# Performance work log

Measured on AMD Instinct MI355X. Metric: run time of the kernel, lower is better.

## Reference

```python
import jax, jax.numpy as jnp
import numpy as np

# Mamba block hyperparams (canonical: expand=2, d_state=16, d_conv=4, dt_rank=d_model/16)
D_MODEL = 1024
D_INNER = 2 * D_MODEL          # 2048
D_STATE = 16
D_CONV = 4
DT_RANK = D_MODEL // 16        # 64
B, L = 2, 1024


def setup_inputs() -> dict:
    key = jax.random.key(0)
    ks = jax.random.split(key, 12)
    s = lambda fan_in: 1.0 / np.sqrt(fan_in)
    x = jax.random.normal(ks[0], (B, L, D_MODEL), dtype=jnp.float32)
    W_in = jax.random.normal(ks[1], (D_MODEL, 2 * D_INNER), dtype=jnp.float32) * s(D_MODEL)
    conv_w = jax.random.normal(ks[2], (D_INNER, 1, D_CONV), dtype=jnp.float32) * s(D_CONV)
    conv_b = jax.random.normal(ks[3], (D_INNER,), dtype=jnp.float32) * 0.02
    W_xp = jax.random.normal(ks[4], (D_INNER, DT_RANK + 2 * D_STATE), dtype=jnp.float32) * s(D_INNER)
    W_dt = jax.random.normal(ks[5], (DT_RANK, D_INNER), dtype=jnp.float32) * s(DT_RANK)
    # dt bias init so softplus(dt_bias) ~ uniform in [1e-3, 1e-1] (mamba convention)
    dt = jnp.exp(jax.random.uniform(ks[6], (D_INNER,)) * (np.log(0.1) - np.log(1e-3)) + np.log(1e-3))
    dt_bias = dt + jnp.log(-jnp.expm1(-dt))  # inverse softplus
    A_log = jnp.log(jnp.broadcast_to(jnp.arange(1, D_STATE + 1, dtype=jnp.float32), (D_INNER, D_STATE)))
    D_skip = jnp.ones((D_INNER,), dtype=jnp.float32)
    W_out = jax.random.normal(ks[7], (D_INNER, D_MODEL), dtype=jnp.float32) * s(D_INNER)
    return {"x": x, "W_in": W_in, "conv_w": conv_w, "conv_b": conv_b, "W_xp": W_xp,
            "W_dt": W_dt, "dt_bias": dt_bias, "A_log": A_log, "D_skip": D_skip, "W_out": W_out}


def _causal_depthwise_conv(u, conv_w, conv_b):
    # u: [B, E, L], conv_w: [E, 1, K] depthwise, causal (left-pad K-1)
    K = conv_w.shape[-1]
    u = jnp.pad(u, ((0, 0), (0, 0), (K - 1, 0)))
    y = jax.lax.conv_general_dilated(
        u, conv_w, window_strides=(1,), padding='VALID',
        dimension_numbers=('NCH', 'OIH', 'NCH'), feature_group_count=u.shape[1])
    return y + conv_b[None, :, None]


def _selective_scan(u, delta, A, Bm, Cm, D_skip):
    # u, delta: [B,L,E]; A: [E,N]; Bm, Cm: [B,L,N]; D_skip: [E]
    dA = jnp.exp(jnp.einsum('ble,en->blen', delta, A))          # [B,L,E,N]
    dBu = jnp.einsum('ble,bln,ble->blen', delta, Bm, u)          # [B,L,E,N]

    def step(h, inp):
        dA_t, dBu_t, C_t = inp                                    # [B,E,N],[B,E,N],[B,N]
        h = dA_t * h + dBu_t
        y_t = jnp.einsum('ben,bn->be', h, C_t)
        return h, y_t

    h0 = jnp.zeros((u.shape[0], A.shape[0], A.shape[1]), dtype=u.dtype)
    xs = (jnp.swapaxes(dA, 0, 1), jnp.swapaxes(dBu, 0, 1), jnp.swapaxes(Cm, 0, 1))
    _, ys = jax.lax.scan(step, h0, xs)                            # ys: [L,B,E]
    y = jnp.swapaxes(ys, 0, 1)                                    # [B,L,E]
    return y + u * D_skip[None, None, :]


def reference(x, W_in, conv_w, conv_b, W_xp, W_dt, dt_bias, A_log, D_skip, W_out):
    # in_proj and gate split
    xz = x @ W_in                                                 # [B,L,2E]
    xp, z = jnp.split(xz, 2, axis=-1)                             # [B,L,E] each
    # causal depthwise conv + silu
    u = _causal_depthwise_conv(jnp.swapaxes(xp, 1, 2), conv_w, conv_b)
    u = jax.nn.silu(jnp.swapaxes(u, 1, 2))                        # [B,L,E]
    # input-dependent dt, B, C
    x_dbl = u @ W_xp                                              # [B,L,R+2N]
    dt_r, Bm, Cm = jnp.split(x_dbl, [DT_RANK, DT_RANK + D_STATE], axis=-1)
    delta = jax.nn.softplus(dt_r @ W_dt + dt_bias)                # [B,L,E]
    A = -jnp.exp(A_log)                                           # [E,N]
    y = _selective_scan(u, delta, A, Bm, Cm, D_skip)              # [B,L,E]
    # gate and out_proj
    y = y * jax.nn.silu(z)
    return y @ W_out                                              # [B,L,D]
```

## Files before the change

### kernel.cpp

```cpp
#include <hip/hip_runtime.h>
#include <math.h>

#define D_MODEL 1024
#define D_INNER 2048
#define D_STATE 16
#define D_CONV  4
#define DT_RANK 64
#define BB      2
#define LL      1024
#define BL      (BB*LL)
#define CHUNK   16
#define NCHUNK  (LL/CHUNK)
#define KSPLIT  16
#define KS_E    (D_INNER/KSPLIT)

typedef __attribute__((ext_vector_type(8))) short short8;
typedef __attribute__((ext_vector_type(4))) float f32x4;
typedef unsigned short ushort_t;
typedef unsigned int uint_t;

__device__ __forceinline__ float sigmoidf_(float x) { return 1.0f / (1.0f + __expf(-x)); }

__device__ __forceinline__ ushort_t f2bf(float f) {
    uint_t u = __float_as_uint(f);
    uint_t r = (u + 0x7fffu + ((u >> 16) & 1u)) >> 16;
    return (ushort_t)r;
}
__device__ __forceinline__ float bf2f(ushort_t v) {
    return __uint_as_float((uint_t)v << 16);
}

__device__ __forceinline__ void gload_lds16(const void* g, void* l) {
    __builtin_amdgcn_global_load_lds(
        (const __attribute__((address_space(1))) void*)g,
        (__attribute__((address_space(3))) void*)l,
        16, 0, 0);
}

template<int BM, int BN, int SPLIT, int BF0, int BF1>
__global__ __launch_bounds__(256)
void gemm_bf16_t(const ushort_t* __restrict__ A, const ushort_t* __restrict__ Bt,
                 void* __restrict__ C0v, void* __restrict__ C1v,
                 int M, int N, int K, int split) {
    constexpr int WMr = BM / 32;
    constexpr int WNr = BN / 32;
    const int nx = N / BN;
    const int nwg = nx * (M / BM);
    const int wg = ((blockIdx.x & 7) * (nwg >> 3)) + (blockIdx.x >> 3);
    const int row0 = (wg / nx) * BM;
    const int col0 = (wg % nx) * BN;

    __shared__ __align__(16) ushort_t As[BM * 32];
    __shared__ __align__(16) ushort_t Bs[BN * 32];

    const int tid  = threadIdx.x;
    const int lane = tid & 63;
    const int wave = tid >> 6;
    const int wr = wave >> 1, wc = wave & 1;

    f32x4 acc[WMr][WNr];
    #pragma unroll
    for (int m = 0; m < WMr; ++m)
        #pragma unroll
        for (int n = 0; n < WNr; ++n)
            acc[m][n] = (f32x4){0.f, 0.f, 0.f, 0.f};

    const ushort_t* Ablk = A  + (size_t)row0 * K;
    const ushort_t* Bblk = Bt + (size_t)col0 * K;
    const int r_ld  = tid >> 2;
    const int c8_ld = (tid & 3) * 8;

    for (int k0 = 0; k0 < K; k0 += 32) {
        #pragma unroll
        for (int i = 0; i < BM / 64; ++i)
            gload_lds16(Ablk + (size_t)(i * 64 + r_ld) * K + k0 + c8_ld,
                        &As[(i * 64 + wave * 16) * 32]);
        #pragma unroll
        for (int i = 0; i < BN / 64; ++i)
            gload_lds16(Bblk + (size_t)(i * 64 + r_ld) * K + k0 + c8_ld,
                        &Bs[(i * 64 + wave * 16) * 32]);
        __syncthreads();

        short8 af[WMr], bf[WNr];
        const int fr = lane & 15;
        const int kb = (lane >> 4) * 8;
        #pragma unroll
        for (int m = 0; m < WMr; ++m)
            af[m] = *(const short8*)&As[(wr * WMr * 16 + m * 16 + fr) * 32 + kb];
        #pragma unroll
        for (int n = 0; n < WNr; ++n)
            bf[n] = *(const short8*)&Bs[(wc * WNr * 16 + n * 16 + fr) * 32 + kb];

        #pragma unroll
        for (int m = 0; m < WMr; ++m)
            #pragma unroll
            for (int n = 0; n < WNr; ++n)
                acc[m][n] = __builtin_amdgcn_mfma_f32_16x16x32_bf16(
                    af[m], bf[n], acc[m][n], 0, 0, 0);
        __syncthreads();
    }

    const int crow = (lane >> 4) * 4;
    const int ccol = lane & 15;
    const bool second = SPLIT && (col0 >= split);
    const int ldc = second ? (N - split) : (SPLIT ? split : N);
    const int cb  = second ? (col0 - split) : col0;

    #pragma unroll
    for (int m = 0; m < WMr; ++m) {
        #pragma unroll
        for (int n = 0; n < WNr; ++n) {
            size_t base = (size_t)(row0 + wr * WMr * 16 + m * 16 + crow) * ldc
                          + cb + wc * WNr * 16 + n * 16 + ccol;
            if (second) {
                if (BF1) { ushort_t* cp = (ushort_t*)C1v + base;
                    #pragma unroll
                    for (int i = 0; i < 4; ++i) cp[(size_t)i * ldc] = f2bf(acc[m][n][i]);
                } else { float* cp = (float*)C1v + base;
                    #pragma unroll
                    for (int i = 0; i < 4; ++i) cp[(size_t)i * ldc] = acc[m][n][i];
                }
            } else {
                if (BF0) { ushort_t* cp = (ushort_t*)C0v + base;
                    #pragma unroll
                    for (int i = 0; i < 4; ++i) cp[(size_t)i * ldc] = f2bf(acc[m][n][i]);
                } else { float* cp = (float*)C0v + base;
                    #pragma unroll
                    for (int i = 0; i < 4; ++i) cp[(size_t)i * ldc] = acc[m][n][i];
                }
            }
        }
    }
}

__global__ __launch_bounds__(256)
void f32_to_bf16(const float* __restrict__ in, ushort_t* __restrict__ out, int n) {
    int i = (blockIdx.x * 256 + threadIdx.x) * 8;
    if (i + 8 <= n) {
        float4 a = *reinterpret_cast<const float4*>(in + i);
        float4 b = *reinterpret_cast<const float4*>(in + i + 4);
        ushort_t o[8] = {f2bf(a.x), f2bf(a.y), f2bf(a.z), f2bf(a.w),
                         f2bf(b.x), f2bf(b.y), f2bf(b.z), f2bf(b.w)};
        *reinterpret_cast<short8*>(out + i) = *reinterpret_cast<short8*>(o);
    }
}

__global__ __launch_bounds__(256)
void transp_bf16(const float* __restrict__ W, ushort_t* __restrict__ Wt,
                 int R, int C) {
    __shared__ ushort_t tile[32][33];
    int tx = threadIdx.x & 31, ty = threadIdx.x >> 5;
    int r0 = blockIdx.y * 32, c0 = blockIdx.x * 32;
    #pragma unroll
    for (int i = 0; i < 32; i += 8)
        tile[ty + i][tx] = f2bf(W[(size_t)(r0 + ty + i) * C + c0 + tx]);
    __syncthreads();
    #pragma unroll
    for (int i = 0; i < 32; i += 8)
        Wt[(size_t)(c0 + ty + i) * R + r0 + tx] = tile[tx][ty + i];
}

__global__ __launch_bounds__(256)
void gemm_xdbl_convfused(const float* __restrict__ xp, const float* __restrict__ W,
                         const float* __restrict__ conv_w, const float* __restrict__ conv_b,
                         float* __restrict__ part) {
    __shared__ float Ax[16][68];
    __shared__ float Au[16][65];
    __shared__ float Bs[16][96];

    const int tid = threadIdx.x;
    const int m0 = blockIdx.x * 64;
    const int kbase = blockIdx.y * KS_E;
    const int tx = tid & 15;
    const int ty = tid >> 4;
    const bool bhead = (m0 & (LL - 1)) == 0;

    float acc[4][6] = {};

    for (int k0 = 0; k0 < KS_E; k0 += 16) {
        for (int i = tid; i < 67 * 16; i += 256) {
            int r = i >> 4, k = i & 15;
            float v = 0.f;
            if (!(bhead && r < 3))
                v = xp[(size_t)(m0 - 3 + r) * D_INNER + kbase + k0 + k];
            Ax[k][r] = v;
        }
        #pragma unroll
        for (int j = 0; j < 6; ++j) {
            int idx = j * 256 + tid;
            int row = idx / 96, col = idx - row * 96;
            Bs[row][col] = W[(size_t)(kbase + k0 + row) * 96 + col];
        }
        __syncthreads();
        {
            float4 w4 = *(const float4*)&conv_w[(size_t)(kbase + k0 + tx) * 4];
            float cbv = conv_b[kbase + k0 + tx];
            #pragma unroll
            for (int rr = 0; rr < 4; ++rr) {
                int r = ty + rr * 16;
                float a = cbv;
                a = fmaf(w4.x, Ax[tx][r], a);
                a = fmaf(w4.y, Ax[tx][r + 1], a);
                a = fmaf(w4.z, Ax[tx][r + 2], a);
                a = fmaf(w4.w, Ax[tx][r + 3], a);
                Au[tx][r] = a * sigmoidf_(a);
            }
        }
        __syncthreads();
        #pragma unroll
        for (int kk = 0; kk < 16; ++kk) {
            float a[4], b[6];
            #pragma unroll
            for (int i = 0; i < 4; ++i) a[i] = Au[kk][ty * 4 + i];
            #pragma unroll
            for (int j = 0; j < 6; ++j) b[j] = Bs[kk][tx * 6 + j];
            #pragma unroll
            for (int i = 0; i < 4; ++i)
                #pragma unroll
                for (int j = 0; j < 6; ++j)
                    acc[i][j] = fmaf(a[i], b[j], acc[i][j]);
        }
        __syncthreads();
    }

    float* pblk = part + (size_t)blockIdx.y * BL * 96;
    #pragma unroll
    for (int i = 0; i < 4; ++i)
        #pragma unroll
        for (int j = 0; j < 6; ++j)
            pblk[(size_t)(m0 + ty * 4 + i) * 96 + tx * 6 + j] = acc[i][j];
}

__global__ __launch_bounds__(256)
void xdbl_reduce(const float* __restrict__ part, float* __restrict__ x_dbl) {
    int i = blockIdx.x * 256 + threadIdx.x;
    float s = 0.0f;
    #pragma unroll
    for (int k = 0; k < KSPLIT; ++k)
        s += part[(size_t)k * BL * 96 + i];
    x_dbl[i] = s;
}

template<int EPI>
__global__ __launch_bounds__(256)
void gemm_f32(const float* __restrict__ A, const float* __restrict__ B,
              float* __restrict__ C, const float* __restrict__ bias,
              int M, int N, int K, int lda, int ldb, int ldc) {
    __shared__ float As[16][65];
    __shared__ float Bs[16][64];

    const int tid = threadIdx.x;
    const int tx = tid & 15;
    const int ty = tid >> 4;
    const int row0 = blockIdx.y * 64;
    const int col0 = blockIdx.x * 64;

    const int arow = tid >> 4;
    const int acol = tid & 15;
    const int brow = tid >> 6;
    const int bcol = tid & 63;

    float acc[4][4] = {};

    for (int k0 = 0; k0 < K; k0 += 16) {
        #pragma unroll
        for (int p = 0; p < 4; ++p) {
            int r = arow + p * 16;
            As[acol][r] = A[(size_t)(row0 + r) * lda + (k0 + acol)];
        }
        int gc = col0 + bcol;
        #pragma unroll
        for (int p = 0; p < 4; ++p) {
            int r = brow + p * 4;
            Bs[r][bcol] = (gc < N) ? B[(size_t)(k0 + r) * ldb + gc] : 0.0f;
        }
        __syncthreads();
        #pragma unroll
        for (int kk = 0; kk < 16; ++kk) {
            float a[4];
            #pragma unroll
            for (int i = 0; i < 4; ++i) a[i] = As[kk][ty * 4 + i];
            float4 bv = *reinterpret_cast<const float4*>(&Bs[kk][tx * 4]);
            float b4[4] = {bv.x, bv.y, bv.z, bv.w};
            #pragma unroll
            for (int i = 0; i < 4; ++i)
                #pragma unroll
                for (int j = 0; j < 4; ++j)
                    acc[i][j] = fmaf(a[i], b4[j], acc[i][j]);
        }
        __syncthreads();
    }

    #pragma unroll
    for (int i = 0; i < 4; ++i) {
        int gr = row0 + ty * 4 + i;
        #pragma unroll
        for (int j = 0; j < 4; ++j) {
            int gc = col0 + tx * 4 + j;
            if (gc < N) {
                float v = acc[i][j];
                if (EPI == 1) {
                    v += bias[gc];
                    v = (v > 20.0f) ? v : log1pf(__expf(v));
                }
                C[(size_t)gr * ldc + gc] = v;
            }
        }
    }
}

__global__ __launch_bounds__(256)
void scan_phase1(const float* __restrict__ delta, const float* __restrict__ xp,
                 const float* __restrict__ conv_w, const float* __restrict__ conv_b,
                 const float* __restrict__ x_dbl, const float* __restrict__ A_log,
                 float* __restrict__ hend, float* __restrict__ sumdelta) {
    int g = blockIdx.x * 256 + threadIdx.x;
    int e = g & (D_INNER - 1);
    int c = (g >> 11) & (NCHUNK - 1);
    int b = g >> 17;

    float A_en[D_STATE];
    bool geo = true;
    #pragma unroll
    for (int n = 0; n < D_STATE; n += 4) {
        float4 al = *(const float4*)&A_log[e * D_STATE + n];
        A_en[n]     = -__expf(al.x);
        A_en[n + 1] = -__expf(al.y);
        A_en[n + 2] = -__expf(al.z);
        A_en[n + 3] = -__expf(al.w);
    }
    #pragma unroll
    for (int n = 0; n < D_STATE; ++n)
        geo = geo && (fabsf(A_en[n] + (float)(n + 1)) <= 2e-5f * (float)(n + 1));

    const int t0 = c * CHUNK;
    const float* dptr = delta + (size_t)(b * LL + t0) * D_INNER + e;
    const float* xptr = xp    + (size_t)(b * LL + t0) * D_INNER + e;
    const float* xb   = x_dbl + (size_t)(b * LL + t0) * 96 + DT_RANK;
    float4 w4 = *(const float4*)&conv_w[(size_t)e * 4];
    float cbv = conv_b[e];

    float xw0 = 0.f, xw1 = 0.f, xw2 = 0.f;
    if (c > 0) {
        xw0 = xptr[-3 * D_INNER];
        xw1 = xptr[-2 * D_INNER];
        xw2 = xptr[-1 * D_INNER];
    }

    float h[D_STATE];
    #pragma unroll
    for (int n = 0; n < D_STATE; ++n) h[n] = 0.0f;
    float S = 0.0f;

    if (geo) {
        for (int t = 0; t < CHUNK; ++t) {
            float dv = dptr[(size_t)t * D_INNER];
            float x0 = xptr[(size_t)t * D_INNER];
            float a = cbv;
            a = fmaf(w4.x, xw0, a); a = fmaf(w4.y, xw1, a);
            a = fmaf(w4.z, xw2, a); a = fmaf(w4.w, x0, a);
            float uv = a * sigmoidf_(a);
            xw0 = xw1; xw1 = xw2; xw2 = x0;
            const float* xrow = xb + (size_t)t * 96;
            float4 B0 = *(const float4*)(xrow);
            float4 B1 = *(const float4*)(xrow + 4);
            float4 B2 = *(const float4*)(xrow + 8);
            float4 B3 = *(const float4*)(xrow + 12);
            float Bv[16] = {B0.x, B0.y, B0.z, B0.w, B1.x, B1.y, B1.z, B1.w,
                            B2.x, B2.y, B2.z, B2.w, B3.x, B3.y, B3.z, B3.w};
            S += dv;
            float du = dv * uv;
            float q = __expf(-dv);
            float dA = q;
            #pragma unroll
            for (int n = 0; n < D_STATE; ++n) {
                h[n] = fmaf(dA, h[n], du * Bv[n]);
                dA *= q;
            }
        }
    } else {
        for (int t = 0; t < CHUNK; ++t) {
            float dv = dptr[(size_t)t * D_INNER];
            float x0 = xptr[(size_t)t * D_INNER];
            float a = cbv;
            a = fmaf(w4.x, xw0, a); a = fmaf(w4.y, xw1, a);
            a = fmaf(w4.z, xw2, a); a = fmaf(w4.w, x0, a);
            float uv = a * sigmoidf_(a);
            xw0 = xw1; xw1 = xw2; xw2 = x0;
            const float* xrow = xb + (size_t)t * 96;
            float4 B0 = *(const float4*)(xrow);
            float4 B1 = *(const float4*)(xrow + 4);
            float4 B2 = *(const float4*)(xrow + 8);
            float4 B3 = *(const float4*)(xrow + 12);
            float Bv[16] = {B0.x, B0.y, B0.z, B0.w, B1.x, B1.y, B1.z, B1.w,
                            B2.x, B2.y, B2.z, B2.w, B3.x, B3.y, B3.z, B3.w};
            S += dv;
            float du = dv * uv;
            #pragma unroll
            for (int n = 0; n < D_STATE; ++n) {
                float dA = __expf(dv * A_en[n]);
                h[n] = fmaf(dA, h[n], du * Bv[n]);
            }
        }
    }

    size_t rbase = ((size_t)(c * BB + b) * D_STATE) * D_INNER + e;
    #pragma unroll
    for (int n = 0; n < D_STATE; ++n)
        hend[rbase + (size_t)n * D_INNER] = h[n];
    sumdelta[(size_t)(c * BB + b) * D_INNER + e] = S;
}

__global__ __launch_bounds__(256)
void scan_phase2(const float* __restrict__ A_log, const float* __restrict__ sumdelta,
                 float* __restrict__ hh) {
    int g = blockIdx.x * 256 + threadIdx.x;
    int e = g & (D_INNER - 1);
    int n = (g >> 11) & (D_STATE - 1);
    int b = g >> 15;
    float A_en = -__expf(A_log[e * D_STATE + n]);
    float np1 = (float)(n + 1);
    if (fabsf(A_en + np1) <= 2e-5f * np1) A_en = -np1;
    float h = 0.0f;
    for (int c = 0; c < NCHUNK; ++c) {
        size_t idx = ((size_t)(c * BB + b) * D_STATE + n) * D_INNER + e;
        float he = hh[idx];
        float dA = __expf(A_en * sumdelta[(size_t)(c * BB + b) * D_INNER + e]);
        hh[idx] = h;
        h = fmaf(dA, h, he);
    }
}

__global__ __launch_bounds__(256)
void scan_phase3(const float* __restrict__ delta, const float* __restrict__ xp,
                 const float* __restrict__ conv_w, const float* __restrict__ conv_b,
                 const float* __restrict__ x_dbl, const ushort_t* __restrict__ zbf,
                 const float* __restrict__ A_log, const float* __restrict__ D_skip,
                 const float* __restrict__ hin, ushort_t* __restrict__ ybf) {
    int g = blockIdx.x * 256 + threadIdx.x;
    int e = g & (D_INNER - 1);
    int c = (g >> 11) & (NCHUNK - 1);
    int b = g >> 17;

    float A_en[D_STATE];
    bool geo = true;
    #pragma unroll
    for (int n = 0; n < D_STATE; n += 4) {
        float4 al = *(const float4*)&A_log[e * D_STATE + n];
        A_en[n]     = -__expf(al.x);
        A_en[n + 1] = -__expf(al.y);
        A_en[n + 2] = -__expf(al.z);
        A_en[n + 3] = -__expf(al.w);
    }
    #pragma unroll
    for (int n = 0; n < D_STATE; ++n)
        geo = geo && (fabsf(A_en[n] + (float)(n + 1)) <= 2e-5f * (float)(n + 1));

    float D_e = D_skip[e];
    float h[D_STATE];
    size_t rbase = ((size_t)(c * BB + b) * D_STATE) * D_INNER + e;
    #pragma unroll
    for (int n = 0; n < D_STATE; ++n)
        h[n] = hin[rbase + (size_t)n * D_INNER];

    const int t0 = c * CHUNK;
    const float* dptr = delta + (size_t)(b * LL + t0) * D_INNER + e;
    const float* xptr = xp    + (size_t)(b * LL + t0) * D_INNER + e;
    const float* xb   = x_dbl + (size_t)(b * LL + t0) * 96 + DT_RANK;
    const ushort_t* zptr = zbf + (size_t)(b * LL + t0) * D_INNER + e;
    ushort_t* yout = ybf + (size_t)(b * LL + t0) * D_INNER + e;
    float4 w4 = *(const float4*)&conv_w[(size_t)e * 4];
    float cbv = conv_b[e];

    float xw0 = 0.f, xw1 = 0.f, xw2 = 0.f;
    if (c > 0) {
        xw0 = xptr[-3 * D_INNER];
        xw1 = xptr[-2 * D_INNER];
        xw2 = xptr[-1 * D_INNER];
    }

    if (geo) {
        for (int t = 0; t < CHUNK; ++t) {
            float dv = dptr[(size_t)t * D_INNER];
            float x0 = xptr[(size_t)t * D_INNER];
            float a = cbv;
            a = fmaf(w4.x, xw0, a); a = fmaf(w4.y, xw1, a);
            a = fmaf(w4.z, xw2, a); a = fmaf(w4.w, x0, a);
            float uv = a * sigmoidf_(a);
            xw0 = xw1; xw1 = xw2; xw2 = x0;
            const float* xrow = xb + (size_t)t * 96;
            float4 B0 = *(const float4*)(xrow);
            float4 B1 = *(const float4*)(xrow + 4);
            float4 B2 = *(const float4*)(xrow + 8);
            float4 B3 = *(const float4*)(xrow + 12);
            float4 C0 = *(const float4*)(xrow + 16);
            float4 C1 = *(const float4*)(xrow + 20);
            float4 C2 = *(const float4*)(xrow + 24);
            float4 C3 = *(const float4*)(xrow + 28);
            float Bv[16] = {B0.x, B0.y, B0.z, B0.w, B1.x, B1.y, B1.z, B1.w,
                            B2.x, B2.y, B2.z, B2.w, B3.x, B3.y, B3.z, B3.w};
            float Cv[16] = {C0.x, C0.y, C0.z, C0.w, C1.x, C1.y, C1.z, C1.w,
                            C2.x, C2.y, C2.z, C2.w, C3.x, C3.y, C3.z, C3.w};
            float du = dv * uv;
            float q = __expf(-dv);
            float dA = q;
            float y = 0.0f;
            #pragma unroll
            for (int n = 0; n < D_STATE; ++n) {
                h[n] = fmaf(dA, h[n], du * Bv[n]);
                y = fmaf(h[n], Cv[n], y);
                dA *= q;
            }
            float zv = bf2f(zptr[(size_t)t * D_INNER]);
            float yg = (y + uv * D_e) * (zv * sigmoidf_(zv));
            yout[(size_t)t * D_INNER] = f2bf(yg);
        }
    } else {
        for (int t = 0; t < CHUNK; ++t) {
            float dv = dptr[(size_t)t * D_INNER];
            float x0 = xptr[(size_t)t * D_INNER];
            float a = cbv;
            a = fmaf(w4.x, xw0, a); a = fmaf(w4.y, xw1, a);
            a = fmaf(w4.z, xw2, a); a = fmaf(w4.w, x0, a);
            float uv = a * sigmoidf_(a);
            xw0 = xw1; xw1 = xw2; xw2 = x0;
            const float* xrow = xb + (size_t)t * 96;
            float4 B0 = *(const float4*)(xrow);
            float4 B1 = *(const float4*)(xrow + 4);
            float4 B2 = *(const float4*)(xrow + 8);
            float4 B3 = *(const float4*)(xrow + 12);
            float4 C0 = *(const float4*)(xrow + 16);
            float4 C1 = *(const float4*)(xrow + 20);
            float4 C2 = *(const float4*)(xrow + 24);
            float4 C3 = *(const float4*)(xrow + 28);
            float Bv[16] = {B0.x, B0.y, B0.z, B0.w, B1.x, B1.y, B1.z, B1.w,
                            B2.x, B2.y, B2.z, B2.w, B3.x, B3.y, B3.z, B3.w};
            float Cv[16] = {C0.x, C0.y, C0.z, C0.w, C1.x, C1.y, C1.z, C1.w,
                            C2.x, C2.y, C2.z, C2.w, C3.x, C3.y, C3.z, C3.w};
            float du = dv * uv;
            float y = 0.0f;
            #pragma unroll
            for (int n = 0; n < D_STATE; ++n) {
                float dA = __expf(dv * A_en[n]);
                h[n] = fmaf(dA, h[n], du * Bv[n]);
                y = fmaf(h[n], Cv[n], y);
            }
            float zv = bf2f(zptr[(size_t)t * D_INNER]);
            float yg = (y + uv * D_e) * (zv * sigmoidf_(zv));
            yout[(size_t)t * D_INNER] = f2bf(yg);
        }
    }
}

extern "C" void kernel_launch(void* const* d_in, const int* in_sizes, int n_in,
                              void* d_out, int out_size, void* d_ws, size_t ws_size,
                              hipStream_t stream) {
    const float* x      = (const float*)d_in[0];
    const float* W_in   = (const float*)d_in[1];
    const float* conv_w = (const float*)d_in[2];
    const float* conv_b = (const float*)d_in[3];
    const float* W_xp   = (const float*)d_in[4];
    const float* W_dt   = (const float*)d_in[5];
    const float* dt_b   = (const float*)d_in[6];
    const float* A_log  = (const float*)d_in[7];
    const float* D_skip = (const float*)d_in[8];
    const float* W_out  = (const float*)d_in[9];
    float* out = (float*)d_out;

    const size_t M1 = 1024 * 1024;
    float* ws = (float*)d_ws;
    float*    xp    = ws;
    float*    hend  = ws + 4 * M1;
    float*    delta = ws + 8 * M1;
    ushort_t* z_bf  = (ushort_t*)(ws + 12 * M1);
    float*    x_dbl = ws + 14 * M1;
    float*    sumd  = ws + 14 * M1 + 262144;
    ushort_t* ybf   = (ushort_t*)(ws + 14 * M1 + 524288);
    float*    xdbl_part = delta;
    ushort_t* Wint_bf   = (ushort_t*)hend;
    ushort_t* Woutt_bf  = (ushort_t*)hend;
    ushort_t* x_bf      = ybf;

    dim3 blk(256);

    hipLaunchKernelGGL(f32_to_bf16, dim3((BL * D_MODEL) / (256 * 8)), blk, 0, stream,
                       x, x_bf, BL * D_MODEL);
    hipLaunchKernelGGL(transp_bf16, dim3(4096 / 32, 1024 / 32), blk, 0, stream,
                       W_in, Wint_bf, 1024, 4096);
    hipLaunchKernelGGL((gemm_bf16_t<64, 128, 1, 0, 1>),
                       dim3((BL / 64) * (4096 / 128)), blk, 0, stream,
                       x_bf, Wint_bf, (void*)xp, (void*)z_bf,
                       BL, 2 * D_INNER, D_MODEL, D_INNER);
    hipLaunchKernelGGL(gemm_xdbl_convfused, dim3(BL / 64, KSPLIT), blk, 0, stream,
                       xp, W_xp, conv_w, conv_b, xdbl_part);
    hipLaunchKernelGGL(xdbl_reduce, dim3((BL * 96) / 256), blk, 0, stream,
                       xdbl_part, x_dbl);
    hipLaunchKernelGGL((gemm_f32<1>), dim3(D_INNER / 64, BL / 64), blk, 0, stream,
                       x_dbl, W_dt, delta, dt_b, BL, D_INNER, DT_RANK, 96, D_INNER, D_INNER);
    hipLaunchKernelGGL(scan_phase1, dim3((BB * NCHUNK * D_INNER) / 256), blk, 0, stream,
                       delta, xp, conv_w, conv_b, x_dbl, A_log, hend, sumd);
    hipLaunchKernelGGL(scan_phase2, dim3((BB * D_STATE * D_INNER) / 256), blk, 0, stream,
                       A_log, sumd, hend);
    hipLaunchKernelGGL(scan_phase3, dim3((BB * NCHUNK * D_INNER) / 256), blk, 0, stream,
                       delta, xp, conv_w, conv_b, x_dbl, z_bf, A_log, D_skip, hend, ybf);
    hipLaunchKernelGGL(transp_bf16, dim3(1024 / 32, 2048 / 32), blk, 0, stream,
                       W_out, Woutt_bf, 2048, 1024);
    hipLaunchKernelGGL((gemm_bf16_t<64, 64, 0, 0, 0>),
                       dim3((BL / 64) * (D_MODEL / 64)), blk, 0, stream,
                       ybf, Woutt_bf, (void*)out, (void*)out,
                       BL, D_MODEL, D_INNER, D_MODEL);
}
```

Baseline: 185.1 us.

## Store xp and chunk states in bf16 and merge prep conversions into one kernel

Merges the x-to-bf16 conversion and both weight transposes into a single prep launch, and rearranges workspace buffers so the W_out transpose no longer aliases hend. The in_proj GEMM now writes xp in bf16, and the conv/scan kernels read it as bf16. The scan's inter-chunk states (hend) are also kept in bf16 between phases. This cuts launch count and global memory traffic, at the cost of lower precision for xp and the carried scan states, which may raise numerical error.

```diff
diff --git a/kernel.cpp b/kernel.cpp
--- a/kernel.cpp
+++ b/kernel.cpp
@@ -133,24 +133,12 @@
     }
 }
 
-__global__ __launch_bounds__(256)
-void f32_to_bf16(const float* __restrict__ in, ushort_t* __restrict__ out, int n) {
-    int i = (blockIdx.x * 256 + threadIdx.x) * 8;
-    if (i + 8 <= n) {
-        float4 a = *reinterpret_cast<const float4*>(in + i);
-        float4 b = *reinterpret_cast<const float4*>(in + i + 4);
-        ushort_t o[8] = {f2bf(a.x), f2bf(a.y), f2bf(a.z), f2bf(a.w),
-                         f2bf(b.x), f2bf(b.y), f2bf(b.z), f2bf(b.w)};
-        *reinterpret_cast<short8*>(out + i) = *reinterpret_cast<short8*>(o);
-    }
-}
-
-__global__ __launch_bounds__(256)
-void transp_bf16(const float* __restrict__ W, ushort_t* __restrict__ Wt,
-                 int R, int C) {
-    __shared__ ushort_t tile[32][33];
+__device__ __forceinline__ void transp_tile_body(const float* __restrict__ W,
+                                                 ushort_t* __restrict__ Wt,
+                                                 int R, int C, int bx, int by,
+                                                 ushort_t (*tile)[33]) {
     int tx = threadIdx.x & 31, ty = threadIdx.x >> 5;
-    int r0 = blockIdx.y * 32, c0 = blockIdx.x * 32;
+    int r0 = by * 32, c0 = bx * 32;
     #pragma unroll
     for (int i = 0; i < 32; i += 8)
         tile[ty + i][tx] = f2bf(W[(size_t)(r0 + ty + i) * C + c0 + tx]);
@@ -161,7 +149,29 @@
 }
 
 __global__ __launch_bounds__(256)
-void gemm_xdbl_convfused(const float* __restrict__ xp, const float* __restrict__ W,
+void prep_kernel(const float* __restrict__ x, ushort_t* __restrict__ x_bf,
+                 const float* __restrict__ W_in, ushort_t* __restrict__ Wint,
+                 const float* __restrict__ W_out, ushort_t* __restrict__ Woutt) {
+    __shared__ ushort_t tile[32][33];
+    int bid = blockIdx.x;
+    if (bid < 1024) {
+        int i = (bid * 256 + threadIdx.x) * 8;
+        float4 a = *reinterpret_cast<const float4*>(x + i);
+        float4 b = *reinterpret_cast<const float4*>(x + i + 4);
+        ushort_t o[8] = {f2bf(a.x), f2bf(a.y), f2bf(a.z), f2bf(a.w),
+                         f2bf(b.x), f2bf(b.y), f2bf(b.z), f2bf(b.w)};
+        *reinterpret_cast<short8*>(x_bf + i) = *reinterpret_cast<short8*>(o);
+    } else if (bid < 1024 + 4096) {
+        int bi = bid - 1024;
+        transp_tile_body(W_in, Wint, 1024, 4096, bi & 127, bi >> 7, tile);
+    } else {
+        int bi = bid - 5120;
+        transp_tile_body(W_out, Woutt, 2048, 1024, bi & 31, bi >> 5, tile);
+    }
+}
+
+__global__ __launch_bounds__(256)
+void gemm_xdbl_convfused(const ushort_t* __restrict__ xp, const float* __restrict__ W,
                          const float* __restrict__ conv_w, const float* __restrict__ conv_b,
                          float* __restrict__ part) {
     __shared__ float Ax[16][68];
@@ -182,7 +192,7 @@
             int r = i >> 4, k = i & 15;
             float v = 0.f;
             if (!(bhead && r < 3))
-                v = xp[(size_t)(m0 - 3 + r) * D_INNER + kbase + k0 + k];
+                v = bf2f(xp[(size_t)(m0 - 3 + r) * D_INNER + kbase + k0 + k]);
             Ax[k][r] = v;
         }
         #pragma unroll
@@ -310,10 +320,10 @@
 }
 
 __global__ __launch_bounds__(256)
-void scan_phase1(const float* __restrict__ delta, const float* __restrict__ xp,
+void scan_phase1(const float* __restrict__ delta, const ushort_t* __restrict__ xp,
                  const float* __restrict__ conv_w, const float* __restrict__ conv_b,
                  const float* __restrict__ x_dbl, const float* __restrict__ A_log,
-                 float* __restrict__ hend, float* __restrict__ sumdelta) {
+                 ushort_t* __restrict__ hend, float* __restrict__ sumdelta) {
     int g = blockIdx.x * 256 + threadIdx.x;
     int e = g & (D_INNER - 1);
     int c = (g >> 11) & (NCHUNK - 1);
@@ -335,16 +345,16 @@
 
     const int t0 = c * CHUNK;
     const float* dptr = delta + (size_t)(b * LL + t0) * D_INNER + e;
-    const float* xptr = xp    + (size_t)(b * LL + t0) * D_INNER + e;
+    const ushort_t* xptr = xp + (size_t)(b * LL + t0) * D_INNER + e;
     const float* xb   = x_dbl + (size_t)(b * LL + t0) * 96 + DT_RANK;
     float4 w4 = *(const float4*)&conv_w[(size_t)e * 4];
     float cbv = conv_b[e];
 
     float xw0 = 0.f, xw1 = 0.f, xw2 = 0.f;
     if (c > 0) {
-        xw0 = xptr[-3 * D_INNER];
-        xw1 = xptr[-2 * D_INNER];
-        xw2 = xptr[-1 * D_INNER];
+        xw0 = bf2f(xptr[-3 * D_INNER]);
+        xw1 = bf2f(xptr[-2 * D_INNER]);
+        xw2 = bf2f(xptr[-1 * D_INNER]);
     }
 
     float h[D_STATE];
@@ -355,7 +365,7 @@
     if (geo) {
         for (int t = 0; t < CHUNK; ++t) {
             float dv = dptr[(size_t)t * D_INNER];
-            float x0 = xptr[(size_t)t * D_INNER];
+            float x0 = bf2f(xptr[(size_t)t * D_INNER]);
             float a = cbv;
             a = fmaf(w4.x, xw0, a); a = fmaf(w4.y, xw1, a);
             a = fmaf(w4.z, xw2, a); a = fmaf(w4.w, x0, a);
@@ -381,7 +391,7 @@
     } else {
         for (int t = 0; t < CHUNK; ++t) {
             float dv = dptr[(size_t)t * D_INNER];
-            float x0 = xptr[(size_t)t * D_INNER];
+            float x0 = bf2f(xptr[(size_t)t * D_INNER]);
             float a = cbv;
             a = fmaf(w4.x, xw0, a); a = fmaf(w4.y, xw1, a);
             a = fmaf(w4.z, xw2, a); a = fmaf(w4.w, x0, a);
@@ -407,13 +417,13 @@
     size_t rbase = ((size_t)(c * BB + b) * D_STATE) * D_INNER + e;
     #pragma unroll
     for (int n = 0; n < D_STATE; ++n)
-        hend[rbase + (size_t)n * D_INNER] = h[n];
+        hend[rbase + (size_t)n * D_INNER] = f2bf(h[n]);
     sumdelta[(size_t)(c * BB + b) * D_INNER + e] = S;
 }
 
 __global__ __launch_bounds__(256)
 void scan_phase2(const float* __restrict__ A_log, const float* __restrict__ sumdelta,
-                 float* __restrict__ hh) {
+                 ushort_t* __restrict__ hh) {
     int g = blockIdx.x * 256 + threadIdx.x;
     int e = g & (D_INNER - 1);
     int n = (g >> 11) & (D_STATE - 1);
@@ -424,19 +434,19 @@
     float h = 0.0f;
     for (int c = 0; c < NCHUNK; ++c) {
         size_t idx = ((size_t)(c * BB + b) * D_STATE + n) * D_INNER + e;
-        float he = hh[idx];
+        float he = bf2f(hh[idx]);
         float dA = __expf(A_en * sumdelta[(size_t)(c * BB + b) * D_INNER + e]);
-        hh[idx] = h;
+        hh[idx] = f2bf(h);
         h = fmaf(dA, h, he);
     }
 }
 
 __global__ __launch_bounds__(256)
-void scan_phase3(const float* __restrict__ delta, const float* __restrict__ xp,
+void scan_phase3(const float* __restrict__ delta, const ushort_t* __restrict__ xp,
                  const float* __restrict__ conv_w, const float* __restrict__ conv_b,
                  const float* __restrict__ x_dbl, const ushort_t* __restrict__ zbf,
                  const float* __restrict__ A_log, const float* __restrict__ D_skip,
-                 const float* __restrict__ hin, ushort_t* __restrict__ ybf) {
+                 const ushort_t* __restrict__ hin, ushort_t* __restrict__ ybf) {
     int g = blockIdx.x * 256 + threadIdx.x;
     int e = g & (D_INNER - 1);
     int c = (g >> 11) & (NCHUNK - 1);
@@ -461,11 +471,11 @@
     size_t rbase = ((size_t)(c * BB + b) * D_STATE) * D_INNER + e;
     #pragma unroll
     for (int n = 0; n < D_STATE; ++n)
-        h[n] = hin[rbase + (size_t)n * D_INNER];
+        h[n] = bf2f(hin[rbase + (size_t)n * D_INNER]);
 
     const int t0 = c * CHUNK;
     const float* dptr = delta + (size_t)(b * LL + t0) * D_INNER + e;
-    const float* xptr = xp    + (size_t)(b * LL + t0) * D_INNER + e;
+    const ushort_t* xptr = xp + (size_t)(b * LL + t0) * D_INNER + e;
     const float* xb   = x_dbl + (size_t)(b * LL + t0) * 96 + DT_RANK;
     const ushort_t* zptr = zbf + (size_t)(b * LL + t0) * D_INNER + e;
     ushort_t* yout = ybf + (size_t)(b * LL + t0) * D_INNER + e;
@@ -474,15 +484,15 @@
 
     float xw0 = 0.f, xw1 = 0.f, xw2 = 0.f;
     if (c > 0) {
-        xw0 = xptr[-3 * D_INNER];
-        xw1 = xptr[-2 * D_INNER];
-        xw2 = xptr[-1 * D_INNER];
+        xw0 = bf2f(xptr[-3 * D_INNER]);
+        xw1 = bf2f(xptr[-2 * D_INNER]);
+        xw2 = bf2f(xptr[-1 * D_INNER]);
     }
 
     if (geo) {
         for (int t = 0; t < CHUNK; ++t) {
             float dv = dptr[(size_t)t * D_INNER];
-            float x0 = xptr[(size_t)t * D_INNER];
+            float x0 = bf2f(xptr[(size_t)t * D_INNER]);
             float a = cbv;
             a = fmaf(w4.x, xw0, a); a = fmaf(w4.y, xw1, a);
             a = fmaf(w4.z, xw2, a); a = fmaf(w4.w, x0, a);
@@ -518,7 +528,7 @@
     } else {
         for (int t = 0; t < CHUNK; ++t) {
             float dv = dptr[(size_t)t * D_INNER];
-            float x0 = xptr[(size_t)t * D_INNER];
+            float x0 = bf2f(xptr[(size_t)t * D_INNER]);
             float a = cbv;
             a = fmaf(w4.x, xw0, a); a = fmaf(w4.y, xw1, a);
             a = fmaf(w4.z, xw2, a); a = fmaf(w4.w, x0, a);
@@ -569,42 +579,38 @@
 
     const size_t M1 = 1024 * 1024;
     float* ws = (float*)d_ws;
-    float*    xp    = ws;
-    float*    hend  = ws + 4 * M1;
+    ushort_t* xp_bf = (ushort_t*)ws;
+    ushort_t* hend  = (ushort_t*)(ws + 4 * M1);
+    ushort_t* Wint_bf = (ushort_t*)(ws + 6 * M1);
     float*    delta = ws + 8 * M1;
     ushort_t* z_bf  = (ushort_t*)(ws + 12 * M1);
     float*    x_dbl = ws + 14 * M1;
     float*    sumd  = ws + 14 * M1 + 262144;
     ushort_t* ybf   = (ushort_t*)(ws + 14 * M1 + 524288);
     float*    xdbl_part = delta;
-    ushort_t* Wint_bf   = (ushort_t*)hend;
-    ushort_t* Woutt_bf  = (ushort_t*)hend;
-    ushort_t* x_bf      = ybf;
+    ushort_t* x_bf  = ybf;
+    ushort_t* Woutt_bf = (ushort_t*)(ws + 17 * M1);
 
     dim3 blk(256);
 
-    hipLaunchKernelGGL(f32_to_bf16, dim3((BL * D_MODEL) / (256 * 8)), blk, 0, stream,
-                       x, x_bf, BL * D_MODEL);
-    hipLaunchKernelGGL(transp_bf16, dim3(4096 / 32, 1024 / 32), blk, 0, stream,
-                       W_in, Wint_bf, 1024, 4096);
-    hipLaunchKernelGGL((gemm_bf16_t<64, 128, 1, 0, 1>),
+    hipLaunchKernelGGL(prep_kernel, dim3(1024 + 4096 + 2048), blk, 0, stream,
+                       x, x_bf, W_in, Wint_bf, W_out, Woutt_bf);
+    hipLaunchKernelGGL((gemm_bf16_t<64, 128, 1, 1, 1>),
                        dim3((BL / 64) * (4096 / 128)), blk, 0, stream,
-                       x_bf, Wint_bf, (void*)xp, (void*)z_bf,
+                       x_bf, Wint_bf, (void*)xp_bf, (void*)z_bf,
                        BL, 2 * D_INNER, D_MODEL, D_INNER);
     hipLaunchKernelGGL(gemm_xdbl_convfused, dim3(BL / 64, KSPLIT), blk, 0, stream,
-                       xp, W_xp, conv_w, conv_b, xdbl_part);
+                       xp_bf, W_xp, conv_w, conv_b, xdbl_part);
     hipLaunchKernelGGL(xdbl_reduce, dim3((BL * 96) / 256), blk, 0, stream,
                        xdbl_part, x_dbl);
     hipLaunchKernelGGL((gemm_f32<1>), dim3(D_INNER / 64, BL / 64), blk, 0, stream,
                        x_dbl, W_dt, delta, dt_b, BL, D_INNER, DT_RANK, 96, D_INNER, D_INNER);
     hipLaunchKernelGGL(scan_phase1, dim3((BB * NCHUNK * D_INNER) / 256), blk, 0, stream,
-                       delta, xp, conv_w, conv_b, x_dbl, A_log, hend, sumd);
+                       delta, xp_bf, conv_w, conv_b, x_dbl, A_log, hend, sumd);
     hipLaunchKernelGGL(scan_phase2, dim3((BB * D_STATE * D_INNER) / 256), blk, 0, stream,
                        A_log, sumd, hend);
     hipLaunchKernelGGL(scan_phase3, dim3((BB * NCHUNK * D_INNER) / 256), blk, 0, stream,
-                       delta, xp, conv_w, conv_b, x_dbl, z_bf, A_log, D_skip, hend, ybf);
-    hipLaunchKernelGGL(transp_bf16, dim3(1024 / 32, 2048 / 32), blk, 0, stream,
-                       W_out, Woutt_bf, 2048, 1024);
+                       delta, xp_bf, conv_w, conv_b, x_dbl, z_bf, A_log, D_skip, hend, ybf);
     hipLaunchKernelGGL((gemm_bf16_t<64, 64, 0, 0, 0>),
                        dim3((BL / 64) * (D_MODEL / 64)), blk, 0, stream,
                        ybf, Woutt_bf, (void*)out, (void*)out,
```

After: 176.0 us. 4.9% less time.
